# Kernel tuning notes

Hardware: AMD Instinct MI355X
Metric: run time of the kernel (lower is better)

The kernel has to match this reference:

```python
import jax, jax.numpy as jnp
import numpy as np

HIDDEN = 16
N_CLASSES = 10
N_NODES = 100000
N_EDGES = 3200000
D_FEAT = 128
NEG_SLOPE = 0.1


def setup_inputs() -> dict:
    key = jax.random.key(0)
    k1, k2, k3 = jax.random.split(key, 3)
    features = jax.random.normal(k1, (N_NODES, D_FEAT), dtype=jnp.float32)
    edge_src = jax.random.randint(k2, (N_EDGES,), 0, N_NODES, dtype=jnp.int64)
    edge_dst = jax.random.randint(k3, (N_EDGES,), 0, N_NODES, dtype=jnp.int64)
    return {"features": features, "edge_src": edge_src, "edge_dst": edge_dst}


def reference(features, edge_src, edge_dst):
    # SpMM: h[v] = sum over edges (u->v) of features[u]   (binary adjacency)
    msgs = features[edge_src]                      # [E, F] irregular gather
    h = jax.ops.segment_sum(msgs, edge_dst, num_segments=N_NODES)  # [N, F]
    # x @ ones(F, HIDDEN): every column equals the row-sum of h
    r1 = jnp.sum(h, axis=-1)                       # [N]
    a1 = jax.nn.leaky_relu(r1, NEG_SLOPE)          # leaky relu, slope 0.1
    # x @ ones(HIDDEN, N_CLASSES): each class column = HIDDEN * a1
    r2 = HIDDEN * a1
    a2 = jax.nn.leaky_relu(r2, NEG_SLOPE)
    # x @ ones(N_CLASSES, 1) then .int() and flatten
    r3 = N_CLASSES * a2                            # [N]
    return r3.astype(jnp.int32).reshape(-1)
```

## Files before the change

kernel.cpp:

```cpp
#include <hip/hip_runtime.h>

#define N_NODES  100000
#define N_EDGES  3200000
#define D_FEAT   128
#define SLICE    33344
#define SLICE4   (SLICE / 4)
#define N_SLICES 3
#define NCHUNK   80
#define EPB      40000
#define EPT      16
#define VEC4     (EPT / 4)
#define TPB      1024
#define STRIDE   (TPB * EPT)

__device__ __forceinline__ unsigned short f2bf(float f) {
    union { float f; unsigned u; } c; c.f = f;
    unsigned r = c.u + 0x7FFFu + ((c.u >> 16) & 1u);
    return (unsigned short)(r >> 16);
}
__device__ __forceinline__ float bf2f(unsigned short h) {
    union { unsigned u; float f; } c; c.u = ((unsigned)h) << 16; return c.f;
}

__global__ void __launch_bounds__(256) rowsum_kernel(
    const float* __restrict__ feat,
    float* __restrict__ rowsum)
{
    const int gid = (int)(blockIdx.x * blockDim.x + threadIdx.x);
    const int row = gid >> 5;
    const int sub = gid & 31;
    if (row >= N_NODES) return;

    const float4 v = reinterpret_cast<const float4*>(
        feat + (size_t)row * D_FEAT)[sub];
    float s = (v.x + v.y) + (v.z + v.w);

    #pragma unroll
    for (int off = 16; off > 0; off >>= 1)
        s += __shfl_xor(s, off, 64);

    if (sub == 0) rowsum[row] = s;
}

struct Stage { int4 d[VEC4]; int4 s[VEC4]; };

__device__ __forceinline__ void load16(Stage& st,
                                       const int* __restrict__ ed,
                                       const int* __restrict__ es,
                                       int e, int end)
{
    if (e < end) {
        #pragma unroll
        for (int q = 0; q < VEC4; ++q) {
            st.d[q] = *reinterpret_cast<const int4*>(ed + e + q * 4);
            st.s[q] = *reinterpret_cast<const int4*>(es + e + q * 4);
        }
    }
}

__device__ __forceinline__ void gather16(const Stage& st, bool valid,
                                         int lo, unsigned len,
                                         const float* __restrict__ rowsum,
                                         unsigned* j, float* w)
{
    #pragma unroll
    for (int q = 0; q < VEC4; ++q) {
        const int dd[4] = { st.d[q].x, st.d[q].y, st.d[q].z, st.d[q].w };
        const int ss[4] = { st.s[q].x, st.s[q].y, st.s[q].z, st.s[q].w };
        #pragma unroll
        for (int t = 0; t < 4; ++t) {
            const unsigned jj = valid ? (unsigned)(dd[t] - lo) : 0xFFFFFFFFu;
            j[q * 4 + t] = jj;
            w[q * 4 + t] = (jj < len) ? rowsum[ss[t]] : 0.0f;
        }
    }
}

__global__ void __launch_bounds__(TPB, 4) scatter_kernel(
    const int* __restrict__ edge_src,
    const int* __restrict__ edge_dst,
    const float* __restrict__ rowsum,
    unsigned short* __restrict__ copies)
{
    __shared__ float lds[SLICE];

    const int tid  = (int)threadIdx.x;
    const int bid  = (int)blockIdx.x;
    const int g    = bid / 24;
    const int r    = bid % 24;
    const int xcd  = r & 7;
    const int s    = r >> 3;
    const int b    = g * 8 + xcd;
    const int lo   = s * SLICE;
    const unsigned len = (unsigned)((N_NODES - lo < SLICE) ? (N_NODES - lo) : SLICE);

    float4 z; z.x = z.y = z.z = z.w = 0.0f;
    for (int i = tid; i < SLICE4; i += TPB)
        reinterpret_cast<float4*>(lds)[i] = z;
    __syncthreads();

    const int begin = b * EPB;
    const int end   = begin + EPB;

    int eA = begin + tid * EPT;
    int eB = eA + STRIDE;

    Stage stA, stB;
    load16(stA, edge_dst, edge_src, eA, end);
    load16(stB, edge_dst, edge_src, eB, end);

    unsigned jA[EPT]; float wA[EPT];
    gather16(stA, eA < end, lo, len, rowsum, jA, wA);

    while (eA < end) {
        const int eC = eB + STRIDE;
        Stage stC;
        load16(stC, edge_dst, edge_src, eC, end);

        unsigned jB[EPT]; float wB[EPT];
        gather16(stB, eB < end, lo, len, rowsum, jB, wB);

        #pragma unroll
        for (int k = 0; k < EPT; ++k)
            if (jA[k] < len) atomicAdd(&lds[jA[k]], wA[k]);

        eA = eB; eB = eC;
        stB = stC;
        #pragma unroll
        for (int k = 0; k < EPT; ++k) { jA[k] = jB[k]; wA[k] = wB[k]; }
    }
    __syncthreads();

    unsigned short* __restrict__ dstp = copies + ((size_t)s * NCHUNK + b) * SLICE;
    const int len4 = (int)len >> 2;
    for (int i = tid; i < len4; i += TPB) {
        const float4 v = reinterpret_cast<const float4*>(lds)[i];
        ushort4 o;
        o.x = f2bf(v.x); o.y = f2bf(v.y); o.z = f2bf(v.z); o.w = f2bf(v.w);
        reinterpret_cast<ushort4*>(dstp)[i] = o;
    }
}

__global__ void __launch_bounds__(256) reduce_final_kernel(
    const unsigned short* __restrict__ copies,
    int* __restrict__ out)
{
    const int i4 = (int)(blockIdx.x * blockDim.x + threadIdx.x);
    if (i4 >= N_NODES / 4) return;

    const int s  = (i4 >= 2 * SLICE4) ? 2 : (i4 >= SLICE4 ? 1 : 0);
    const int j4 = i4 - s * SLICE4;

    float ax = 0.0f, ay = 0.0f, az = 0.0f, aw = 0.0f;
    const ushort4* base = reinterpret_cast<const ushort4*>(copies)
                        + (size_t)s * NCHUNK * SLICE4 + j4;
    #pragma unroll 4
    for (int c = 0; c < NCHUNK; ++c) {
        const ushort4 v = base[(size_t)c * SLICE4];
        ax += bf2f(v.x); ay += bf2f(v.y); az += bf2f(v.z); aw += bf2f(v.w);
    }

    auto act = [](float x) -> int {
        const float a1 = (x  > 0.0f) ? x  : 0.1f * x;
        const float r2 = 16.0f * a1;
        const float a2 = (r2 > 0.0f) ? r2 : 0.1f * r2;
        return (int)(10.0f * a2);
    };

    int4 o;
    o.x = act(ax); o.y = act(ay); o.z = act(az); o.w = act(aw);
    reinterpret_cast<int4*>(out)[i4] = o;
}

extern "C" void kernel_launch(void* const* d_in, const int* in_sizes, int n_in,
                              void* d_out, int out_size, void* d_ws, size_t ws_size,
                              hipStream_t stream)
{
    const float* feat     = (const float*)d_in[0];
    const int*   edge_src = (const int*)d_in[1];
    const int*   edge_dst = (const int*)d_in[2];
    int*         out      = (int*)d_out;

    float* rowsum = (float*)d_ws;
    unsigned short* copies = (unsigned short*)(rowsum + N_NODES);

    {
        const int threads = 256;
        const long long total = (long long)N_NODES * 32;
        const int blocks = (int)((total + threads - 1) / threads);
        rowsum_kernel<<<blocks, threads, 0, stream>>>(feat, rowsum);
    }

    scatter_kernel<<<N_SLICES * NCHUNK, TPB, 0, stream>>>(edge_src, edge_dst,
                                                          rowsum, copies);

    {
        const int threads = 256;
        const int blocks = (N_NODES / 4 + threads - 1) / threads;
        reduce_final_kernel<<<blocks, threads, 0, stream>>>(copies, out);
    }
}
```

Before: 55.35 us.

## Split scatter into five smaller LDS slices with lighter per-thread pipelining

Shrinks the shared-memory histogram slice from about 33K to 20K nodes (5 slices instead of 3), which allows more resident blocks per CU (launch bounds raised to 8). Per-thread work is halved to 8 edges with a single-stage prefetch instead of a two-stage 16-edge pipeline, which cuts register pressure. The trade-off is that each edge is read 5 times instead of 3, so edge-index traffic grows, and the reduce pass now has more copies to sum.

New measurement: 52.17 us. -5.7%, faster.

```diff
diff --git a/kernel.cpp b/kernel.cpp
--- a/kernel.cpp
+++ b/kernel.cpp
@@ -3,13 +3,12 @@
 #define N_NODES  100000
 #define N_EDGES  3200000
 #define D_FEAT   128
-#define SLICE    33344
+#define SLICE    20000
 #define SLICE4   (SLICE / 4)
-#define N_SLICES 3
+#define N_SLICES 5
 #define NCHUNK   80
 #define EPB      40000
-#define EPT      16
-#define VEC4     (EPT / 4)
+#define EPT      8
 #define TPB      1024
 #define STRIDE   (TPB * EPT)
 
@@ -42,41 +41,7 @@
     if (sub == 0) rowsum[row] = s;
 }
 
-struct Stage { int4 d[VEC4]; int4 s[VEC4]; };
-
-__device__ __forceinline__ void load16(Stage& st,
-                                       const int* __restrict__ ed,
-                                       const int* __restrict__ es,
-                                       int e, int end)
-{
-    if (e < end) {
-        #pragma unroll
-        for (int q = 0; q < VEC4; ++q) {
-            st.d[q] = *reinterpret_cast<const int4*>(ed + e + q * 4);
-            st.s[q] = *reinterpret_cast<const int4*>(es + e + q * 4);
-        }
-    }
-}
-
-__device__ __forceinline__ void gather16(const Stage& st, bool valid,
-                                         int lo, unsigned len,
-                                         const float* __restrict__ rowsum,
-                                         unsigned* j, float* w)
-{
-    #pragma unroll
-    for (int q = 0; q < VEC4; ++q) {
-        const int dd[4] = { st.d[q].x, st.d[q].y, st.d[q].z, st.d[q].w };
-        const int ss[4] = { st.s[q].x, st.s[q].y, st.s[q].z, st.s[q].w };
-        #pragma unroll
-        for (int t = 0; t < 4; ++t) {
-            const unsigned jj = valid ? (unsigned)(dd[t] - lo) : 0xFFFFFFFFu;
-            j[q * 4 + t] = jj;
-            w[q * 4 + t] = (jj < len) ? rowsum[ss[t]] : 0.0f;
-        }
-    }
-}
-
-__global__ void __launch_bounds__(TPB, 4) scatter_kernel(
+__global__ void __launch_bounds__(TPB, 8) scatter_kernel(
     const int* __restrict__ edge_src,
     const int* __restrict__ edge_dst,
     const float* __restrict__ rowsum,
@@ -84,15 +49,14 @@
 {
     __shared__ float lds[SLICE];
 
-    const int tid  = (int)threadIdx.x;
-    const int bid  = (int)blockIdx.x;
-    const int g    = bid / 24;
-    const int r    = bid % 24;
-    const int xcd  = r & 7;
-    const int s    = r >> 3;
-    const int b    = g * 8 + xcd;
-    const int lo   = s * SLICE;
-    const unsigned len = (unsigned)((N_NODES - lo < SLICE) ? (N_NODES - lo) : SLICE);
+    const int tid = (int)threadIdx.x;
+    const int bid = (int)blockIdx.x;
+    const int g   = bid / 40;
+    const int r   = bid % 40;
+    const int xcd = r & 7;
+    const int s   = r >> 3;
+    const int b   = g * 8 + xcd;
+    const int lo  = s * SLICE;
 
     float4 z; z.x = z.y = z.z = z.w = 0.0f;
     for (int i = tid; i < SLICE4; i += TPB)
@@ -102,41 +66,61 @@
     const int begin = b * EPB;
     const int end   = begin + EPB;
 
-    int eA = begin + tid * EPT;
-    int eB = eA + STRIDE;
+    int e = begin + tid * EPT;
+    bool v = (e < end);
 
-    Stage stA, stB;
-    load16(stA, edge_dst, edge_src, eA, end);
-    load16(stB, edge_dst, edge_src, eB, end);
+    int4 d0, d1, s0, s1;
+    if (v) {
+        d0 = *(const int4*)(edge_dst + e);     s0 = *(const int4*)(edge_src + e);
+        d1 = *(const int4*)(edge_dst + e + 4); s1 = *(const int4*)(edge_src + e + 4);
+    }
 
-    unsigned jA[EPT]; float wA[EPT];
-    gather16(stA, eA < end, lo, len, rowsum, jA, wA);
+    while (v) {
+        const int en = e + STRIDE;
+        const bool vn = (en < end);
+        int4 nd0, nd1, ns0, ns1;
+        if (vn) {
+            nd0 = *(const int4*)(edge_dst + en);     ns0 = *(const int4*)(edge_src + en);
+            nd1 = *(const int4*)(edge_dst + en + 4); ns1 = *(const int4*)(edge_src + en + 4);
+        }
 
-    while (eA < end) {
-        const int eC = eB + STRIDE;
-        Stage stC;
-        load16(stC, edge_dst, edge_src, eC, end);
+        const unsigned j0 = (unsigned)(d0.x - lo);
+        const unsigned j1 = (unsigned)(d0.y - lo);
+        const unsigned j2 = (unsigned)(d0.z - lo);
+        const unsigned j3 = (unsigned)(d0.w - lo);
+        const unsigned j4 = (unsigned)(d1.x - lo);
+        const unsigned j5 = (unsigned)(d1.y - lo);
+        const unsigned j6 = (unsigned)(d1.z - lo);
+        const unsigned j7 = (unsigned)(d1.w - lo);
 
-        unsigned jB[EPT]; float wB[EPT];
-        gather16(stB, eB < end, lo, len, rowsum, jB, wB);
+        float w0 = (j0 < SLICE) ? rowsum[s0.x] : 0.0f;
+        float w1 = (j1 < SLICE) ? rowsum[s0.y] : 0.0f;
+        float w2 = (j2 < SLICE) ? rowsum[s0.z] : 0.0f;
+        float w3 = (j3 < SLICE) ? rowsum[s0.w] : 0.0f;
+        float w4 = (j4 < SLICE) ? rowsum[s1.x] : 0.0f;
+        float w5 = (j5 < SLICE) ? rowsum[s1.y] : 0.0f;
+        float w6 = (j6 < SLICE) ? rowsum[s1.z] : 0.0f;
+        float w7 = (j7 < SLICE) ? rowsum[s1.w] : 0.0f;
 
-        #pragma unroll
-        for (int k = 0; k < EPT; ++k)
-            if (jA[k] < len) atomicAdd(&lds[jA[k]], wA[k]);
+        if (j0 < SLICE) atomicAdd(&lds[j0], w0);
+        if (j1 < SLICE) atomicAdd(&lds[j1], w1);
+        if (j2 < SLICE) atomicAdd(&lds[j2], w2);
+        if (j3 < SLICE) atomicAdd(&lds[j3], w3);
+        if (j4 < SLICE) atomicAdd(&lds[j4], w4);
+        if (j5 < SLICE) atomicAdd(&lds[j5], w5);
+        if (j6 < SLICE) atomicAdd(&lds[j6], w6);
+        if (j7 < SLICE) atomicAdd(&lds[j7], w7);
 
-        eA = eB; eB = eC;
-        stB = stC;
-        #pragma unroll
-        for (int k = 0; k < EPT; ++k) { jA[k] = jB[k]; wA[k] = wB[k]; }
+        e = en; v = vn;
+        d0 = nd0; d1 = nd1; s0 = ns0; s1 = ns1;
     }
     __syncthreads();
 
     unsigned short* __restrict__ dstp = copies + ((size_t)s * NCHUNK + b) * SLICE;
-    const int len4 = (int)len >> 2;
-    for (int i = tid; i < len4; i += TPB) {
-        const float4 v = reinterpret_cast<const float4*>(lds)[i];
+    for (int i = tid; i < SLICE4; i += TPB) {
+        const float4 vv = reinterpret_cast<const float4*>(lds)[i];
         ushort4 o;
-        o.x = f2bf(v.x); o.y = f2bf(v.y); o.z = f2bf(v.z); o.w = f2bf(v.w);
+        o.x = f2bf(vv.x); o.y = f2bf(vv.y); o.z = f2bf(vv.z); o.w = f2bf(vv.w);
         reinterpret_cast<ushort4*>(dstp)[i] = o;
     }
 }
@@ -148,7 +132,7 @@
     const int i4 = (int)(blockIdx.x * blockDim.x + threadIdx.x);
     if (i4 >= N_NODES / 4) return;
 
-    const int s  = (i4 >= 2 * SLICE4) ? 2 : (i4 >= SLICE4 ? 1 : 0);
+    const int s  = i4 / SLICE4;
     const int j4 = i4 - s * SLICE4;
 
     float ax = 0.0f, ay = 0.0f, az = 0.0f, aw = 0.0f;
```
